# Kernel optimization log

Hardware: AMD Instinct MI355X
Metric: run time of the kernel (lower is better)

## Reference

```python
import jax, jax.numpy as jnp
import numpy as np
import math

B, N, L = 1, 256, 384
D_MSA, D_PAIR, H, DH = 256, 128, 8, 32


def layer_norm(x, g, b, eps=1e-5):
    m = jnp.mean(x, axis=-1, keepdims=True)
    v = jnp.var(x, axis=-1, keepdims=True)
    return (x - m) * jax.lax.rsqrt(v + eps) * g + b


def setup_inputs() -> dict:
    key = jax.random.key(0)
    ks = jax.random.split(key, 16)
    hd = H * DH
    w = lambda k, shp, s=0.05: (jax.random.normal(k, shp, dtype=jnp.float32) * s)
    return {
        "msa": jax.random.normal(ks[0], (B, N, L, D_MSA), dtype=jnp.float32),
        "pair": jax.random.normal(ks[1], (B, L, L, D_PAIR), dtype=jnp.float32),
        "ln_msa_g": jnp.ones((D_MSA,), jnp.float32),
        "ln_msa_b": jnp.zeros((D_MSA,), jnp.float32),
        "ln_pair_g": jnp.ones((D_PAIR,), jnp.float32),
        "ln_pair_b": jnp.zeros((D_PAIR,), jnp.float32),
        "sw_q_w": w(ks[2], (D_MSA, hd)),
        "sw_q_b": jnp.zeros((hd,), jnp.float32),
        "sw_k_w": w(ks[3], (D_MSA, hd)),
        "sw_k_b": jnp.zeros((hd,), jnp.float32),
        "wq": w(ks[4], (D_MSA, hd)),
        "wk": w(ks[5], (D_MSA, hd)),
        "wv": w(ks[6], (D_MSA, hd)),
        "wb": w(ks[7], (D_PAIR, H)),
        "wg": w(ks[8], (D_MSA, hd)),
        "bg": jnp.ones((hd,), jnp.float32),
        "wo": w(ks[9], (hd, D_MSA)),
        "bo": jnp.zeros((D_MSA,), jnp.float32),
    }


def reference(msa, pair, ln_msa_g, ln_msa_b, ln_pair_g, ln_pair_b,
              sw_q_w, sw_q_b, sw_k_w, sw_k_b,
              wq, wk, wv, wb, wg, bg, wo, bo):
    b, n, l, _ = msa.shape
    scale = 1.0 / math.sqrt(DH)

    msa_n = layer_norm(msa, ln_msa_g, ln_msa_b)
    pair_n = layer_norm(pair, ln_pair_g, ln_pair_b)

    # SequenceWeight: attention of target seq (row 0) over all N rows, per (L, head)
    tar = msa_n[:, 0]                                       # [B,L,D]
    swq = (tar @ sw_q_w + sw_q_b).reshape(b, l, H, DH) * scale
    swk = (msa_n @ sw_k_w + sw_k_b).reshape(b, n, l, H, DH)
    sw_logits = jnp.einsum('blhd,bnlhd->bnlh', swq, swk)    # [B,N,L,H]
    seq_weight = jax.nn.softmax(sw_logits, axis=1)          # softmax over N (dropout: eval)

    query = (msa_n @ wq).reshape(b, n, l, H, DH) * seq_weight[..., None]
    key = (msa_n @ wk).reshape(b, n, l, H, DH) * scale
    value = (msa_n @ wv).reshape(b, n, l, H, DH)
    bias = pair_n @ wb                                      # [B,L,L,H]
    gate = jax.nn.sigmoid(msa_n @ wg + bg)                  # [B,N,L,H*DH]

    attn = jnp.einsum('bsqhd,bskhd->bqkh', query, key) + bias
    attn = jax.nn.softmax(attn, axis=-2)                    # over k axis
    out = jnp.einsum('bqkh,bskhd->bsqhd', attn, value).reshape(b, n, l, H * DH)
    out = gate * out
    return out @ wo + bo
```

## Files before the change

### kernel.cpp

```cpp
#include <hip/hip_runtime.h>
#include <hip/hip_fp16.h>
#include <stdint.h>

#define NSEQ 256
#define LSEQ 384
#define DM   256
#define DP   128
#define NH   8
#define DHD  32
#define NL   (NSEQ*LSEQ)
#define LL   (LSEQ*LSEQ)
#define SCALE 0.17677669529663687f

typedef unsigned short u16;
typedef short bf16x8 __attribute__((ext_vector_type(8)));
typedef float f32x4 __attribute__((ext_vector_type(4)));

__device__ __forceinline__ float b2f(u16 s){
  union { uint32_t u; float f; } v; v.u = ((uint32_t)s)<<16; return v.f;
}
__device__ __forceinline__ u16 f2b(float f){
  union { float f; uint32_t u; } v; v.f = f;
  uint32_t u = v.u;
  return (u16)((u + 0x7FFFu + ((u>>16)&1u)) >> 16);
}
__device__ __forceinline__ float wsum(float x){
  #pragma unroll
  for(int o=32;o>0;o>>=1) x += __shfl_xor(x,o,64);
  return x;
}
__device__ __forceinline__ float wmax(float x){
  #pragma unroll
  for(int o=32;o>0;o>>=1) x = fmaxf(x, __shfl_xor(x,o,64));
  return x;
}
__device__ __forceinline__ void gload16(const void* g, void* l){
  __builtin_amdgcn_global_load_lds((const __attribute__((address_space(1))) void*)g,
      (__attribute__((address_space(3))) void*)l, 16, 0, 0);
}

__global__ __launch_bounds__(256) void k_ln_msa(const float* __restrict__ msa,
    const float* __restrict__ g, const float* __restrict__ b, u16* __restrict__ out){
  int lane = threadIdx.x & 63;
  int64_t row = (int64_t)blockIdx.x*4 + (threadIdx.x>>6);
  const float4 x = *(const float4*)(msa + row*DM + lane*4);
  float s = x.x+x.y+x.z+x.w;
  float q = x.x*x.x+x.y*x.y+x.z*x.z+x.w*x.w;
  s = wsum(s); q = wsum(q);
  float mean = s*(1.0f/DM);
  float rstd = rsqrtf(q*(1.0f/DM) - mean*mean + 1e-5f);
  int c = lane*4;
  float4 gv = *(const float4*)(g+c);
  float4 bv = *(const float4*)(b+c);
  ushort4 o;
  o.x=f2b((x.x-mean)*rstd*gv.x+bv.x);
  o.y=f2b((x.y-mean)*rstd*gv.y+bv.y);
  o.z=f2b((x.z-mean)*rstd*gv.z+bv.z);
  o.w=f2b((x.w-mean)*rstd*gv.w+bv.w);
  *(ushort4*)(out + row*DM + c) = o;
}

__global__ __launch_bounds__(256) void k_wconv(const float* __restrict__ wq,
    const float* __restrict__ wk, const float* __restrict__ wv,
    const float* __restrict__ wg, const float* __restrict__ wo,
    u16* __restrict__ WTall, u16* __restrict__ WOT){
  __shared__ float tile[64][65];
  int z = blockIdx.z;
  const float* src = (z==0)?wq:(z==1)?wk:(z==2)?wv:(z==3)?wg:wo;
  u16* dst = (z<4) ? (WTall + z*DM*DM) : WOT;
  int k0 = blockIdx.x*64, n0 = blockIdx.y*64, t = threadIdx.x;
  int r = t>>4, c4 = (t&15)*4;
  #pragma unroll
  for(int it=0; it<4; it++){
    float4 v = *(const float4*)(src + (int64_t)(k0 + it*16 + r)*DM + n0 + c4);
    tile[it*16+r][c4+0]=v.x; tile[it*16+r][c4+1]=v.y;
    tile[it*16+r][c4+2]=v.z; tile[it*16+r][c4+3]=v.w;
  }
  __syncthreads();
  #pragma unroll
  for(int it=0; it<4; it++){
    int nl = it*16 + r, kl = c4;
    ushort4 o;
    o.x=f2b(tile[kl+0][nl]); o.y=f2b(tile[kl+1][nl]);
    o.z=f2b(tile[kl+2][nl]); o.w=f2b(tile[kl+3][nl]);
    *(ushort4*)(dst + (int64_t)(n0+nl)*DM + k0 + kl) = o;
  }
}

__global__ __launch_bounds__(256) void k_u(const u16* __restrict__ msa_n,
    const float* __restrict__ sw_q_w, const float* __restrict__ sw_q_b,
    const float* __restrict__ sw_k_w, float* __restrict__ u){
  __shared__ float tar[DM];
  __shared__ float swq[DM];
  int l = blockIdx.x, t = threadIdx.x;
  tar[t] = b2f(msa_n[(int64_t)l*DM + t]);
  __syncthreads();
  float acc = sw_q_b[t];
  for(int c=0;c<DM;c++) acc += tar[c]*sw_q_w[c*DM + t];
  swq[t] = acc * SCALE;
  __syncthreads();
  float res[NH];
  #pragma unroll
  for(int h=0;h<NH;h++){
    float a = 0.f;
    #pragma unroll
    for(int d=0;d<DHD;d+=4){
      float4 w = *(const float4*)(sw_k_w + t*DM + h*DHD + d);
      a += w.x*swq[h*DHD+d] + w.y*swq[h*DHD+d+1] + w.z*swq[h*DHD+d+2] + w.w*swq[h*DHD+d+3];
    }
    res[h]=a;
  }
  #pragma unroll
  for(int h=0;h<NH;h++) u[((int64_t)l*NH + h)*DM + t] = res[h];
}

__global__ __launch_bounds__(256) void k_seqw(const u16* __restrict__ msa_n,
    const float* __restrict__ u, float* __restrict__ sw){
  __shared__ float ul[NH*DM];
  __shared__ float lg[NH*256];
  __shared__ float mx[NH], sm[NH];
  int l = blockIdx.x, t = threadIdx.x;
  #pragma unroll
  for(int h=0;h<NH;h++) ul[h*DM+t] = u[((int64_t)l*NH+h)*DM + t];
  __syncthreads();
  float acc[NH] = {};
  const u16* row = msa_n + ((int64_t)t*LSEQ + l)*DM;
  for(int c=0;c<DM;c+=4){
    ushort4 xv = *(const ushort4*)(row + c);
    float x0=b2f(xv.x), x1=b2f(xv.y), x2=b2f(xv.z), x3=b2f(xv.w);
    #pragma unroll
    for(int h=0;h<NH;h++)
      acc[h] += x0*ul[h*DM+c] + x1*ul[h*DM+c+1] + x2*ul[h*DM+c+2] + x3*ul[h*DM+c+3];
  }
  #pragma unroll
  for(int h=0;h<NH;h++) lg[h*256+t] = acc[h];
  __syncthreads();
  int wv = t>>6, ln = t&63;
  for(int h=wv; h<NH; h+=4){
    float a=lg[h*256+ln], b=lg[h*256+ln+64], c=lg[h*256+ln+128], d=lg[h*256+ln+192];
    float m = wmax(fmaxf(fmaxf(a,b),fmaxf(c,d)));
    float e = __expf(a-m)+__expf(b-m)+__expf(c-m)+__expf(d-m);
    e = wsum(e);
    if(ln==0){ mx[h]=m; sm[h]=1.f/e; }
  }
  __syncthreads();
  float o[NH];
  #pragma unroll
  for(int h=0;h<NH;h++) o[h] = __expf(acc[h]-mx[h])*sm[h];
  float* dst = sw + ((int64_t)t*LSEQ + l)*NH;
  *(float4*)dst     = make_float4(o[0],o[1],o[2],o[3]);
  *(float4*)(dst+4) = make_float4(o[4],o[5],o[6],o[7]);
}

__global__ __launch_bounds__(256) void k_bias(const float* __restrict__ pair,
    const float* __restrict__ g, const float* __restrict__ b,
    const float* __restrict__ wb, float* __restrict__ bias){
  int64_t row = (int64_t)blockIdx.x*256 + threadIdx.x;
  const float* pr = pair + row*DP;
  uint2 xs[32];
  float s = 0.f, q = 0.f;
  #pragma unroll
  for(int i=0;i<32;i++){
    float4 v = *(const float4*)(pr + i*4);
    s += v.x+v.y+v.z+v.w;
    q += v.x*v.x+v.y*v.y+v.z*v.z+v.w*v.w;
    __half2 p0 = __floats2half2_rn(v.x, v.y);
    __half2 p1 = __floats2half2_rn(v.z, v.w);
    xs[i].x = *(const uint32_t*)&p0;
    xs[i].y = *(const uint32_t*)&p1;
  }
  float mean = s*(1.f/DP);
  float rstd = rsqrtf(q*(1.f/DP) - mean*mean + 1e-5f);
  float acc[NH] = {};
  #pragma unroll
  for(int i=0;i<32;i++){
    __half2 p0 = *(const __half2*)&xs[i].x;
    __half2 p1 = *(const __half2*)&xs[i].y;
    float2 f0 = __half22float2(p0);
    float2 f1 = __half22float2(p1);
    float xv[4] = {f0.x, f0.y, f1.x, f1.y};
    #pragma unroll
    for(int c4=0;c4<4;c4++){
      int c = i*4 + c4;
      float y = (xv[c4]-mean)*rstd*g[c] + b[c];
      #pragma unroll
      for(int h=0;h<NH;h++) acc[h] += y*wb[c*NH+h];
    }
  }
  #pragma unroll
  for(int h=0;h<NH;h++) bias[(int64_t)h*LL + row] = acc[h];
}


__global__ __launch_bounds__(256) void k_projf(const u16* __restrict__ A,
    const u16* __restrict__ WT, u16* __restrict__ qb, u16* __restrict__ kb,
    u16* __restrict__ gbuf, u16* __restrict__ VT,
    const float* __restrict__ sw, const float* __restrict__ bg){
  __shared__ short As[128*64];
  __shared__ short Bs[128*64];
  int t = threadIdx.x;
  int w = t>>6, lane = t&63, ln15 = lane&15, quad = lane>>4;
  int rIn = lane>>3, cch = lane&7;
  int mw = (w>>1)*64, nw = (w&1)*64;
  int bx = blockIdx.x;
  int64_t r0 = (int64_t)bx*128;
  int g = cch ^ rIn;
  for(int nt=0; nt<8; nt++){
    int n0 = nt*128;
    f32x4 acc[4][4] = {};
    for(int it=0; it<4; it++){
      int k0 = it*64;
      __syncthreads();
      #pragma unroll
      for(int ti=0; ti<4; ti++){
        int row = w*32 + ti*8 + rIn;
        gload16(A  + (r0+row)*DM + k0 + g*8, &As[(w*32+ti*8)*64]);
        gload16(WT + (int64_t)(n0+row)*DM + k0 + g*8, &Bs[(w*32+ti*8)*64]);
      }
      __syncthreads();
      #pragma unroll
      for(int kk=0;kk<2;kk++){
        int p = (kk*4+quad) ^ (lane&7);
        bf16x8 af[4], bfv[4];
        #pragma unroll
        for(int i=0;i<4;i++) af[i]  = *(const bf16x8*)&As[(mw+i*16+ln15)*64 + p*8];
        #pragma unroll
        for(int j=0;j<4;j++) bfv[j] = *(const bf16x8*)&Bs[(nw+j*16+ln15)*64 + p*8];
        #pragma unroll
        for(int i=0;i<4;i++)
          #pragma unroll
          for(int j=0;j<4;j++)
            acc[i][j] = __builtin_amdgcn_mfma_f32_16x16x32_bf16(af[i], bfv[j], acc[i][j], 0,0,0);
      }
    }
    int mode = nt>>1;
    int cmb = (nt&1)*128 + nw;
    if(mode==2){
      int s = bx/3, kb3 = (bx%3)*128 + mw;
      #pragma unroll
      for(int j=0;j<4;j++){
        int cm = cmb + j*16 + ln15;
        int hh = cm>>5, d = cm&31;
        #pragma unroll
        for(int i=0;i<4;i++){
          int kpos0 = kb3 + i*16 + quad*4;
          ushort4 o;
          o.x=f2b(acc[i][j][0]); o.y=f2b(acc[i][j][1]);
          o.z=f2b(acc[i][j][2]); o.w=f2b(acc[i][j][3]);
          *(ushort4*)(VT + ((int64_t)(hh*NSEQ+s)*DHD + d)*LSEQ + kpos0) = o;
        }
      }
    } else {
      u16* dst = (mode==0)?qb:(mode==1)?kb:gbuf;
      float bgv[4];
      if(mode==3){
        #pragma unroll
        for(int j=0;j<4;j++) bgv[j] = bg[cmb + j*16 + ln15];
      }
      #pragma unroll
      for(int i=0;i<4;i++)
        #pragma unroll
        for(int reg=0;reg<4;reg++){
          int64_t r = r0 + mw + i*16 + quad*4 + reg;
          #pragma unroll
          for(int j=0;j<4;j++){
            int cm = cmb + j*16 + ln15;
            float v = acc[i][j][reg];
            if(mode==0)      v *= sw[r*NH + (cm>>5)];
            else if(mode==1) v *= SCALE;
            else             v = 1.f/(1.f+__expf(-(v+bgv[j])));
            dst[r*DM + cm] = f2b(v);
          }
        }
    }
  }
}

__global__ __launch_bounds__(256) void k_scores(const u16* __restrict__ Q,
    const u16* __restrict__ K, float* __restrict__ scores){
  __shared__ short As[128*64];
  __shared__ short Bs[128*64];
  int t = threadIdx.x;
  int w = t>>6, lane = t&63, ln15 = lane&15, quad = lane>>4;
  int rIn = lane>>3, cch = lane&7;
  int mw = (w>>1)*64, nw = (w&1)*64;
  int q0 = blockIdx.x*128, k0t = blockIdx.y*128;
  int h = blockIdx.z>>2, sc = blockIdx.z&3;
  int g = cch ^ rIn;
  int s_off = g>>2, d16 = g&3;
  f32x4 acc[4][4] = {};
  for(int i2=0; i2<32; i2++){
    int sb = sc*64 + i2*2 + s_off;
    __syncthreads();
    #pragma unroll
    for(int ti=0; ti<4; ti++){
      int row = w*32 + ti*8 + rIn;
      gload16(Q + ((int64_t)sb*LSEQ + q0 + row)*DM + h*DHD + d16*8, &As[(w*32+ti*8)*64]);
      gload16(K + ((int64_t)sb*LSEQ + k0t + row)*DM + h*DHD + d16*8, &Bs[(w*32+ti*8)*64]);
    }
    __syncthreads();
    #pragma unroll
    for(int kk=0;kk<2;kk++){
      int p = (kk*4+quad) ^ (lane&7);
      bf16x8 af[4], bfv[4];
      #pragma unroll
      for(int i=0;i<4;i++) af[i]  = *(const bf16x8*)&As[(mw+i*16+ln15)*64 + p*8];
      #pragma unroll
      for(int j=0;j<4;j++) bfv[j] = *(const bf16x8*)&Bs[(nw+j*16+ln15)*64 + p*8];
      #pragma unroll
      for(int i=0;i<4;i++)
        #pragma unroll
        for(int j=0;j<4;j++)
          acc[i][j] = __builtin_amdgcn_mfma_f32_16x16x32_bf16(af[i], bfv[j], acc[i][j], 0,0,0);
    }
  }
  int64_t slab = (int64_t)sc*NH*LL;
  #pragma unroll
  for(int i=0;i<4;i++)
    #pragma unroll
    for(int reg=0;reg<4;reg++){
      int q = q0 + mw + i*16 + quad*4 + reg;
      float* rp = scores + slab + ((int64_t)h*LSEQ + q)*LSEQ + k0t + nw + ln15;
      #pragma unroll
      for(int j=0;j<4;j++) rp[j*16] = acc[i][j][reg];
    }
}

__global__ __launch_bounds__(128) void k_softmax(const float* __restrict__ scores,
    const float* __restrict__ bias, u16* __restrict__ Pb){
  int hq = blockIdx.x, t = threadIdx.x;
  int64_t base = (int64_t)hq*LSEQ;
  float v[3];
  #pragma unroll
  for(int i=0;i<3;i++){
    int k = t + i*128;
    float x = bias[base+k];
    x += scores[base+k];
    x += scores[(int64_t)1*NH*LL + base + k];
    x += scores[(int64_t)2*NH*LL + base + k];
    x += scores[(int64_t)3*NH*LL + base + k];
    v[i]=x;
  }
  __shared__ float red[2], red2[2];
  int wv=t>>6, ln=t&63;
  float m = fmaxf(fmaxf(v[0],v[1]),v[2]);
  m = wmax(m);
  if(ln==0) red[wv]=m;
  __syncthreads();
  m = fmaxf(red[0],red[1]);
  float e = __expf(v[0]-m)+__expf(v[1]-m)+__expf(v[2]-m);
  e = wsum(e);
  if(ln==0) red2[wv]=e;
  __syncthreads();
  float inv = 1.f/(red2[0]+red2[1]);
  #pragma unroll
  for(int i=0;i<3;i++) Pb[base + t + i*128] = f2b(__expf(v[i]-m)*inv);
}

__global__ __launch_bounds__(256) void k_pv(const u16* __restrict__ VT,
    const u16* __restrict__ Pb, const u16* __restrict__ gbuf,
    u16* __restrict__ attn){
  __shared__ short As[128*64];
  __shared__ short Bs[128*64];
  int t = threadIdx.x;
  int w = t>>6, lane = t&63, ln15 = lane&15, quad = lane>>4;
  int rIn = lane>>3, cch = lane&7;
  int mw = (w>>1)*64, nw = (w&1)*64;
  int mx = blockIdx.x, ny = blockIdx.y, h = blockIdx.z;
  int g = cch ^ rIn;
  f32x4 acc[4][4] = {};
  for(int it=0; it<6; it++){
    int k0 = it*64;
    __syncthreads();
    #pragma unroll
    for(int ti=0; ti<4; ti++){
      int row = w*32 + ti*8 + rIn;
      gload16(VT + ((int64_t)h*8192 + mx*128 + row)*LSEQ + k0 + g*8, &As[(w*32+ti*8)*64]);
      gload16(Pb + ((int64_t)h*LSEQ + ny*128 + row)*LSEQ + k0 + g*8, &Bs[(w*32+ti*8)*64]);
    }
    __syncthreads();
    #pragma unroll
    for(int kk=0;kk<2;kk++){
      int p = (kk*4+quad) ^ (lane&7);
      bf16x8 af[4], bfv[4];
      #pragma unroll
      for(int i=0;i<4;i++) af[i]  = *(const bf16x8*)&As[(mw+i*16+ln15)*64 + p*8];
      #pragma unroll
      for(int j=0;j<4;j++) bfv[j] = *(const bf16x8*)&Bs[(nw+j*16+ln15)*64 + p*8];
      #pragma unroll
      for(int i=0;i<4;i++)
        #pragma unroll
        for(int j=0;j<4;j++)
          acc[i][j] = __builtin_amdgcn_mfma_f32_16x16x32_bf16(af[i], bfv[j], acc[i][j], 0,0,0);
    }
  }
  #pragma unroll
  for(int i=0;i<4;i++){
    int m0 = mx*128 + mw + i*16 + quad*4;
    int s = m0>>5, d0 = m0&31;
    #pragma unroll
    for(int j=0;j<4;j++){
      int q = ny*128 + nw + j*16 + ln15;
      int64_t base = ((int64_t)s*LSEQ + q)*DM + h*DHD + d0;
      ushort4 gv = *(const ushort4*)(gbuf + base);
      ushort4 o;
      o.x = f2b(acc[i][j][0]*b2f(gv.x));
      o.y = f2b(acc[i][j][1]*b2f(gv.y));
      o.z = f2b(acc[i][j][2]*b2f(gv.z));
      o.w = f2b(acc[i][j][3]*b2f(gv.w));
      *(ushort4*)(attn + base) = o;
    }
  }
}

__global__ __launch_bounds__(256) void k_final(const u16* __restrict__ A,
    const u16* __restrict__ WOT, const float* __restrict__ bo,
    float* __restrict__ out){
  __shared__ short As[128*64];
  __shared__ short Bs[128*64];
  int t = threadIdx.x;
  int w = t>>6, lane = t&63, ln15 = lane&15, quad = lane>>4;
  int rIn = lane>>3, cch = lane&7;
  int mw = (w>>1)*64, nw = (w&1)*64;
  int n0 = blockIdx.x*128;
  int64_t r0 = (int64_t)blockIdx.y*128;
  int g = cch ^ rIn;
  f32x4 acc[4][4] = {};
  for(int it=0; it<4; it++){
    int k0 = it*64;
    __syncthreads();
    #pragma unroll
    for(int ti=0; ti<4; ti++){
      int row = w*32 + ti*8 + rIn;
      gload16(A   + (r0+row)*DM + k0 + g*8, &As[(w*32+ti*8)*64]);
      gload16(WOT + (int64_t)(n0+row)*DM + k0 + g*8, &Bs[(w*32+ti*8)*64]);
    }
    __syncthreads();
    #pragma unroll
    for(int kk=0;kk<2;kk++){
      int p = (kk*4+quad) ^ (lane&7);
      bf16x8 af[4], bfv[4];
      #pragma unroll
      for(int i=0;i<4;i++) af[i]  = *(const bf16x8*)&As[(mw+i*16+ln15)*64 + p*8];
      #pragma unroll
      for(int j=0;j<4;j++) bfv[j] = *(const bf16x8*)&Bs[(nw+j*16+ln15)*64 + p*8];
      #pragma unroll
      for(int i=0;i<4;i++)
        #pragma unroll
        for(int j=0;j<4;j++)
          acc[i][j] = __builtin_amdgcn_mfma_f32_16x16x32_bf16(af[i], bfv[j], acc[i][j], 0,0,0);
    }
  }
  float bv[4];
  #pragma unroll
  for(int j=0;j<4;j++) bv[j] = bo[n0 + nw + j*16 + ln15];
  #pragma unroll
  for(int i=0;i<4;i++)
    #pragma unroll
    for(int reg=0;reg<4;reg++){
      int64_t r = r0 + mw + i*16 + quad*4 + reg;
      float* rp = out + r*DM + n0 + nw + ln15;
      #pragma unroll
      for(int j=0;j<4;j++) rp[j*16] = acc[i][j][reg] + bv[j];
    }
}

extern "C" void kernel_launch(void* const* d_in, const int* in_sizes, int n_in,
                              void* d_out, int out_size, void* d_ws, size_t ws_size,
                              hipStream_t stream){
  const float* msa    = (const float*)d_in[0];
  const float* pair   = (const float*)d_in[1];
  const float* lmg    = (const float*)d_in[2];
  const float* lmb    = (const float*)d_in[3];
  const float* lpg    = (const float*)d_in[4];
  const float* lpb    = (const float*)d_in[5];
  const float* sw_q_w = (const float*)d_in[6];
  const float* sw_q_b = (const float*)d_in[7];
  const float* sw_k_w = (const float*)d_in[8];
  const float* wq     = (const float*)d_in[10];
  const float* wk     = (const float*)d_in[11];
  const float* wv     = (const float*)d_in[12];
  const float* wb     = (const float*)d_in[13];
  const float* wg     = (const float*)d_in[14];
  const float* bg     = (const float*)d_in[15];
  const float* wo     = (const float*)d_in[16];
  const float* bo     = (const float*)d_in[17];
  float* out = (float*)d_out;

  u16* msa_n = (u16*)d_ws;
  u16* qb    = msa_n + (int64_t)NL*DM;
  u16* kb    = qb + (int64_t)NL*DM;
  u16* gbuf  = kb + (int64_t)NL*DM;
  u16* VT    = gbuf + (int64_t)NL*DM;
  u16* Pb    = VT + (int64_t)NL*DM;
  u16* WTall = Pb + (int64_t)NH*LSEQ*LSEQ;
  u16* WOT   = WTall + 1024*DM;
  float* u_buf = (float*)(WOT + DM*DM);
  float* sw  = u_buf + (int64_t)LSEQ*NH*DM;
  float* bias = sw + (int64_t)NL*NH;
  float* scores = bias + (int64_t)NH*LL;
  u16* attnout = msa_n;

  k_ln_msa<<<NL/4, 256, 0, stream>>>(msa, lmg, lmb, msa_n);
  k_wconv<<<dim3(4,4,5), 256, 0, stream>>>(wq, wk, wv, wg, wo, WTall, WOT);
  k_u<<<LSEQ, 256, 0, stream>>>(msa_n, sw_q_w, sw_q_b, sw_k_w, u_buf);
  k_seqw<<<LSEQ, 256, 0, stream>>>(msa_n, u_buf, sw);
  k_bias<<<LL/256, 256, 0, stream>>>(pair, lpg, lpb, wb, bias);
  k_projf<<<dim3(NL/128), 256, 0, stream>>>(msa_n, WTall, qb, kb, gbuf, VT, sw, bg);
  k_scores<<<dim3(3,3,32), 256, 0, stream>>>(qb, kb, scores);
  k_softmax<<<NH*LSEQ, 128, 0, stream>>>(scores, bias, Pb);
  k_pv<<<dim3(64,3,NH), 256, 0, stream>>>(VT, Pb, gbuf, attnout);
  k_final<<<dim3(2, NL/128), 256, 0, stream>>>(attnout, WOT, bo, out);
}
```

Baseline: 730.2 us.

## Double-buffer LDS tiles in all MFMA GEMM kernels to overlap loads with compute

Gives the projection, scores, PV and final-output GEMM kernels two LDS buffers per operand. Each kernel issues the global-to-LDS loads for the next k-step before running the MFMAs on the current one, which removes one barrier per iteration. In the projection kernel the nested n-tile/k loops are flattened into one 32-step stream so prefetching also crosses n-tile boundaries, with the epilogue done every fourth step. LDS use per block doubles to 64 KB, which can lower the number of resident blocks per CU.

```diff
diff --git a/kernel.cpp b/kernel.cpp
--- a/kernel.cpp
+++ b/kernel.cpp
@@ -196,8 +196,8 @@
     const u16* __restrict__ WT, u16* __restrict__ qb, u16* __restrict__ kb,
     u16* __restrict__ gbuf, u16* __restrict__ VT,
     const float* __restrict__ sw, const float* __restrict__ bg){
-  __shared__ short As[128*64];
-  __shared__ short Bs[128*64];
+  __shared__ short As[2][128*64];
+  __shared__ short Bs[2][128*64];
   int t = threadIdx.x;
   int w = t>>6, lane = t&63, ln15 = lane&15, quad = lane>>4;
   int rIn = lane>>3, cch = lane&7;
@@ -205,81 +205,92 @@
   int bx = blockIdx.x;
   int64_t r0 = (int64_t)bx*128;
   int g = cch ^ rIn;
-  for(int nt=0; nt<8; nt++){
-    int n0 = nt*128;
-    f32x4 acc[4][4] = {};
-    for(int it=0; it<4; it++){
-      int k0 = it*64;
-      __syncthreads();
-      #pragma unroll
-      for(int ti=0; ti<4; ti++){
-        int row = w*32 + ti*8 + rIn;
-        gload16(A  + (r0+row)*DM + k0 + g*8, &As[(w*32+ti*8)*64]);
-        gload16(WT + (int64_t)(n0+row)*DM + k0 + g*8, &Bs[(w*32+ti*8)*64]);
-      }
-      __syncthreads();
-      #pragma unroll
-      for(int kk=0;kk<2;kk++){
-        int p = (kk*4+quad) ^ (lane&7);
-        bf16x8 af[4], bfv[4];
-        #pragma unroll
-        for(int i=0;i<4;i++) af[i]  = *(const bf16x8*)&As[(mw+i*16+ln15)*64 + p*8];
-        #pragma unroll
-        for(int j=0;j<4;j++) bfv[j] = *(const bf16x8*)&Bs[(nw+j*16+ln15)*64 + p*8];
+
+  auto PSTAGE = [&](int r, int bsel){
+    int n0_ = (r>>2)*128, k0_ = (r&3)*64;
+    #pragma unroll
+    for(int ti=0; ti<4; ti++){
+      int row = w*32 + ti*8 + rIn;
+      gload16(A  + (r0+row)*DM + k0_ + g*8, &As[bsel][(w*32+ti*8)*64]);
+      gload16(WT + (int64_t)(n0_+row)*DM + k0_ + g*8, &Bs[bsel][(w*32+ti*8)*64]);
+    }
+  };
+
+  f32x4 acc[4][4] = {};
+  PSTAGE(0, 0);
+  __syncthreads();
+  for(int r=0; r<32; r++){
+    int buf = r&1;
+    if(r<31) PSTAGE(r+1, buf^1);
+    #pragma unroll
+    for(int kk=0;kk<2;kk++){
+      int p = (kk*4+quad) ^ (lane&7);
+      bf16x8 af[4], bfv[4];
+      #pragma unroll
+      for(int i=0;i<4;i++) af[i]  = *(const bf16x8*)&As[buf][(mw+i*16+ln15)*64 + p*8];
+      #pragma unroll
+      for(int j=0;j<4;j++) bfv[j] = *(const bf16x8*)&Bs[buf][(nw+j*16+ln15)*64 + p*8];
+      #pragma unroll
+      for(int i=0;i<4;i++)
+        #pragma unroll
+        for(int j=0;j<4;j++)
+          acc[i][j] = __builtin_amdgcn_mfma_f32_16x16x32_bf16(af[i], bfv[j], acc[i][j], 0,0,0);
+    }
+    if((r&3)==3){
+      int nt = r>>2;
+      int mode = nt>>1;
+      int cmb = (nt&1)*128 + nw;
+      if(mode==2){
+        int s = bx/3, kb3 = (bx%3)*128 + mw;
+        #pragma unroll
+        for(int j=0;j<4;j++){
+          int cm = cmb + j*16 + ln15;
+          int hh = cm>>5, d = cm&31;
+          #pragma unroll
+          for(int i=0;i<4;i++){
+            int kpos0 = kb3 + i*16 + quad*4;
+            ushort4 o;
+            o.x=f2b(acc[i][j][0]); o.y=f2b(acc[i][j][1]);
+            o.z=f2b(acc[i][j][2]); o.w=f2b(acc[i][j][3]);
+            *(ushort4*)(VT + ((int64_t)(hh*NSEQ+s)*DHD + d)*LSEQ + kpos0) = o;
+          }
+        }
+      } else {
+        u16* dst = (mode==0)?qb:(mode==1)?kb:gbuf;
+        float bgv[4];
+        if(mode==3){
+          #pragma unroll
+          for(int j=0;j<4;j++) bgv[j] = bg[cmb + j*16 + ln15];
+        }
         #pragma unroll
         for(int i=0;i<4;i++)
           #pragma unroll
-          for(int j=0;j<4;j++)
-            acc[i][j] = __builtin_amdgcn_mfma_f32_16x16x32_bf16(af[i], bfv[j], acc[i][j], 0,0,0);
+          for(int reg=0;reg<4;reg++){
+            int64_t rr = r0 + mw + i*16 + quad*4 + reg;
+            #pragma unroll
+            for(int j=0;j<4;j++){
+              int cm = cmb + j*16 + ln15;
+              float v = acc[i][j][reg];
+              if(mode==0)      v *= sw[rr*NH + (cm>>5)];
+              else if(mode==1) v *= SCALE;
+              else             v = 1.f/(1.f+__expf(-(v+bgv[j])));
+              dst[rr*DM + cm] = f2b(v);
+            }
+          }
       }
-    }
-    int mode = nt>>1;
-    int cmb = (nt&1)*128 + nw;
-    if(mode==2){
-      int s = bx/3, kb3 = (bx%3)*128 + mw;
-      #pragma unroll
-      for(int j=0;j<4;j++){
-        int cm = cmb + j*16 + ln15;
-        int hh = cm>>5, d = cm&31;
-        #pragma unroll
-        for(int i=0;i<4;i++){
-          int kpos0 = kb3 + i*16 + quad*4;
-          ushort4 o;
-          o.x=f2b(acc[i][j][0]); o.y=f2b(acc[i][j][1]);
-          o.z=f2b(acc[i][j][2]); o.w=f2b(acc[i][j][3]);
-          *(ushort4*)(VT + ((int64_t)(hh*NSEQ+s)*DHD + d)*LSEQ + kpos0) = o;
-        }
-      }
-    } else {
-      u16* dst = (mode==0)?qb:(mode==1)?kb:gbuf;
-      float bgv[4];
-      if(mode==3){
-        #pragma unroll
-        for(int j=0;j<4;j++) bgv[j] = bg[cmb + j*16 + ln15];
-      }
       #pragma unroll
       for(int i=0;i<4;i++)
         #pragma unroll
-        for(int reg=0;reg<4;reg++){
-          int64_t r = r0 + mw + i*16 + quad*4 + reg;
-          #pragma unroll
-          for(int j=0;j<4;j++){
-            int cm = cmb + j*16 + ln15;
-            float v = acc[i][j][reg];
-            if(mode==0)      v *= sw[r*NH + (cm>>5)];
-            else if(mode==1) v *= SCALE;
-            else             v = 1.f/(1.f+__expf(-(v+bgv[j])));
-            dst[r*DM + cm] = f2b(v);
-          }
-        }
-    }
+        for(int j=0;j<4;j++) acc[i][j] = (f32x4){0.f,0.f,0.f,0.f};
+    }
+    __syncthreads();
   }
 }
 
 __global__ __launch_bounds__(256) void k_scores(const u16* __restrict__ Q,
     const u16* __restrict__ K, float* __restrict__ scores){
-  __shared__ short As[128*64];
-  __shared__ short Bs[128*64];
+  __shared__ short As[2][128*64];
+  __shared__ short Bs[2][128*64];
   int t = threadIdx.x;
   int w = t>>6, lane = t&63, ln15 = lane&15, quad = lane>>4;
   int rIn = lane>>3, cch = lane&7;
@@ -288,31 +299,38 @@
   int h = blockIdx.z>>2, sc = blockIdx.z&3;
   int g = cch ^ rIn;
   int s_off = g>>2, d16 = g&3;
-  f32x4 acc[4][4] = {};
-  for(int i2=0; i2<32; i2++){
+
+  auto PSTAGE = [&](int i2, int bsel){
     int sb = sc*64 + i2*2 + s_off;
-    __syncthreads();
     #pragma unroll
     for(int ti=0; ti<4; ti++){
       int row = w*32 + ti*8 + rIn;
-      gload16(Q + ((int64_t)sb*LSEQ + q0 + row)*DM + h*DHD + d16*8, &As[(w*32+ti*8)*64]);
-      gload16(K + ((int64_t)sb*LSEQ + k0t + row)*DM + h*DHD + d16*8, &Bs[(w*32+ti*8)*64]);
-    }
-    __syncthreads();
+      gload16(Q + ((int64_t)sb*LSEQ + q0 + row)*DM + h*DHD + d16*8, &As[bsel][(w*32+ti*8)*64]);
+      gload16(K + ((int64_t)sb*LSEQ + k0t + row)*DM + h*DHD + d16*8, &Bs[bsel][(w*32+ti*8)*64]);
+    }
+  };
+
+  f32x4 acc[4][4] = {};
+  PSTAGE(0, 0);
+  __syncthreads();
+  for(int i2=0; i2<32; i2++){
+    int buf = i2&1;
+    if(i2<31) PSTAGE(i2+1, buf^1);
     #pragma unroll
     for(int kk=0;kk<2;kk++){
       int p = (kk*4+quad) ^ (lane&7);
       bf16x8 af[4], bfv[4];
       #pragma unroll
-      for(int i=0;i<4;i++) af[i]  = *(const bf16x8*)&As[(mw+i*16+ln15)*64 + p*8];
-      #pragma unroll
-      for(int j=0;j<4;j++) bfv[j] = *(const bf16x8*)&Bs[(nw+j*16+ln15)*64 + p*8];
+      for(int i=0;i<4;i++) af[i]  = *(const bf16x8*)&As[buf][(mw+i*16+ln15)*64 + p*8];
+      #pragma unroll
+      for(int j=0;j<4;j++) bfv[j] = *(const bf16x8*)&Bs[buf][(nw+j*16+ln15)*64 + p*8];
       #pragma unroll
       for(int i=0;i<4;i++)
         #pragma unroll
         for(int j=0;j<4;j++)
           acc[i][j] = __builtin_amdgcn_mfma_f32_16x16x32_bf16(af[i], bfv[j], acc[i][j], 0,0,0);
     }
+    __syncthreads();
   }
   int64_t slab = (int64_t)sc*NH*LL;
   #pragma unroll
@@ -360,39 +378,46 @@
 __global__ __launch_bounds__(256) void k_pv(const u16* __restrict__ VT,
     const u16* __restrict__ Pb, const u16* __restrict__ gbuf,
     u16* __restrict__ attn){
-  __shared__ short As[128*64];
-  __shared__ short Bs[128*64];
+  __shared__ short As[2][128*64];
+  __shared__ short Bs[2][128*64];
   int t = threadIdx.x;
   int w = t>>6, lane = t&63, ln15 = lane&15, quad = lane>>4;
   int rIn = lane>>3, cch = lane&7;
   int mw = (w>>1)*64, nw = (w&1)*64;
   int mx = blockIdx.x, ny = blockIdx.y, h = blockIdx.z;
   int g = cch ^ rIn;
-  f32x4 acc[4][4] = {};
-  for(int it=0; it<6; it++){
+
+  auto PSTAGE = [&](int it, int bsel){
     int k0 = it*64;
-    __syncthreads();
     #pragma unroll
     for(int ti=0; ti<4; ti++){
       int row = w*32 + ti*8 + rIn;
-      gload16(VT + ((int64_t)h*8192 + mx*128 + row)*LSEQ + k0 + g*8, &As[(w*32+ti*8)*64]);
-      gload16(Pb + ((int64_t)h*LSEQ + ny*128 + row)*LSEQ + k0 + g*8, &Bs[(w*32+ti*8)*64]);
-    }
-    __syncthreads();
+      gload16(VT + ((int64_t)h*8192 + mx*128 + row)*LSEQ + k0 + g*8, &As[bsel][(w*32+ti*8)*64]);
+      gload16(Pb + ((int64_t)h*LSEQ + ny*128 + row)*LSEQ + k0 + g*8, &Bs[bsel][(w*32+ti*8)*64]);
+    }
+  };
+
+  f32x4 acc[4][4] = {};
+  PSTAGE(0, 0);
+  __syncthreads();
+  for(int it=0; it<6; it++){
+    int buf = it&1;
+    if(it<5) PSTAGE(it+1, buf^1);
     #pragma unroll
     for(int kk=0;kk<2;kk++){
       int p = (kk*4+quad) ^ (lane&7);
       bf16x8 af[4], bfv[4];
       #pragma unroll
-      for(int i=0;i<4;i++) af[i]  = *(const bf16x8*)&As[(mw+i*16+ln15)*64 + p*8];
-      #pragma unroll
-      for(int j=0;j<4;j++) bfv[j] = *(const bf16x8*)&Bs[(nw+j*16+ln15)*64 + p*8];
+      for(int i=0;i<4;i++) af[i]  = *(const bf16x8*)&As[buf][(mw+i*16+ln15)*64 + p*8];
+      #pragma unroll
+      for(int j=0;j<4;j++) bfv[j] = *(const bf16x8*)&Bs[buf][(nw+j*16+ln15)*64 + p*8];
       #pragma unroll
       for(int i=0;i<4;i++)
         #pragma unroll
         for(int j=0;j<4;j++)
           acc[i][j] = __builtin_amdgcn_mfma_f32_16x16x32_bf16(af[i], bfv[j], acc[i][j], 0,0,0);
     }
+    __syncthreads();
   }
   #pragma unroll
   for(int i=0;i<4;i++){
@@ -416,8 +441,8 @@
 __global__ __launch_bounds__(256) void k_final(const u16* __restrict__ A,
     const u16* __restrict__ WOT, const float* __restrict__ bo,
     float* __restrict__ out){
-  __shared__ short As[128*64];
-  __shared__ short Bs[128*64];
+  __shared__ short As[2][128*64];
+  __shared__ short Bs[2][128*64];
   int t = threadIdx.x;
   int w = t>>6, lane = t&63, ln15 = lane&15, quad = lane>>4;
   int rIn = lane>>3, cch = lane&7;
@@ -425,31 +450,38 @@
   int n0 = blockIdx.x*128;
   int64_t r0 = (int64_t)blockIdx.y*128;
   int g = cch ^ rIn;
-  f32x4 acc[4][4] = {};
-  for(int it=0; it<4; it++){
+
+  auto PSTAGE = [&](int it, int bsel){
     int k0 = it*64;
-    __syncthreads();
     #pragma unroll
     for(int ti=0; ti<4; ti++){
       int row = w*32 + ti*8 + rIn;
-      gload16(A   + (r0+row)*DM + k0 + g*8, &As[(w*32+ti*8)*64]);
-      gload16(WOT + (int64_t)(n0+row)*DM + k0 + g*8, &Bs[(w*32+ti*8)*64]);
-    }
-    __syncthreads();
+      gload16(A   + (r0+row)*DM + k0 + g*8, &As[bsel][(w*32+ti*8)*64]);
+      gload16(WOT + (int64_t)(n0+row)*DM + k0 + g*8, &Bs[bsel][(w*32+ti*8)*64]);
+    }
+  };
+
+  f32x4 acc[4][4] = {};
+  PSTAGE(0, 0);
+  __syncthreads();
+  for(int it=0; it<4; it++){
+    int buf = it&1;
+    if(it<3) PSTAGE(it+1, buf^1);
     #pragma unroll
     for(int kk=0;kk<2;kk++){
       int p = (kk*4+quad) ^ (lane&7);
       bf16x8 af[4], bfv[4];
       #pragma unroll
-      for(int i=0;i<4;i++) af[i]  = *(const bf16x8*)&As[(mw+i*16+ln15)*64 + p*8];
-      #pragma unroll
-      for(int j=0;j<4;j++) bfv[j] = *(const bf16x8*)&Bs[(nw+j*16+ln15)*64 + p*8];
+      for(int i=0;i<4;i++) af[i]  = *(const bf16x8*)&As[buf][(mw+i*16+ln15)*64 + p*8];
+      #pragma unroll
+      for(int j=0;j<4;j++) bfv[j] = *(const bf16x8*)&Bs[buf][(nw+j*16+ln15)*64 + p*8];
       #pragma unroll
       for(int i=0;i<4;i++)
         #pragma unroll
         for(int j=0;j<4;j++)
           acc[i][j] = __builtin_amdgcn_mfma_f32_16x16x32_bf16(af[i], bfv[j], acc[i][j], 0,0,0);
     }
+    __syncthreads();
   }
   float bv[4];
   #pragma unroll
```

New measurement: 758.8 us. 1.04x slower.

## Keep full-K activation tile resident in LDS and stream weights from global

Applied to the files above, without the earlier changes.

In both the projection GEMM and the final output GEMM, the whole 128x256 activation tile is loaded into shared memory once per block with an XOR swizzle. Weight fragments are then read directly from global/L2 into registers, which removes the per-K-step LDS staging and barriers. The final GEMM now loops over both 128-wide N tiles inside one block, so the activation tile is read once instead of twice. The cost is 64KB of LDS per block, which may lower occupancy, and weight loads become uncoalesced 16-byte global reads with no LDS reuse.

```diff
diff --git a/kernel.cpp b/kernel.cpp
--- a/kernel.cpp
+++ b/kernel.cpp
@@ -196,42 +196,45 @@
     const u16* __restrict__ WT, u16* __restrict__ qb, u16* __restrict__ kb,
     u16* __restrict__ gbuf, u16* __restrict__ VT,
     const float* __restrict__ sw, const float* __restrict__ bg){
-  __shared__ short As[128*64];
-  __shared__ short Bs[128*64];
+  __shared__ short As[128*256];
   int t = threadIdx.x;
   int w = t>>6, lane = t&63, ln15 = lane&15, quad = lane>>4;
-  int rIn = lane>>3, cch = lane&7;
   int mw = (w>>1)*64, nw = (w&1)*64;
   int bx = blockIdx.x;
   int64_t r0 = (int64_t)bx*128;
-  int g = cch ^ rIn;
+
+  {
+    int rowl = lane>>5;
+    int pc = lane&31;
+    #pragma unroll
+    for(int m=0;m<16;m++){
+      int q = w*16+m;
+      int row = 2*q + rowl;
+      int gch = pc ^ (row&7);
+      gload16(A + (r0+row)*DM + gch*8, &As[q*512]);
+    }
+  }
+  __syncthreads();
+
   for(int nt=0; nt<8; nt++){
     int n0 = nt*128;
     f32x4 acc[4][4] = {};
-    for(int it=0; it<4; it++){
-      int k0 = it*64;
-      __syncthreads();
-      #pragma unroll
-      for(int ti=0; ti<4; ti++){
-        int row = w*32 + ti*8 + rIn;
-        gload16(A  + (r0+row)*DM + k0 + g*8, &As[(w*32+ti*8)*64]);
-        gload16(WT + (int64_t)(n0+row)*DM + k0 + g*8, &Bs[(w*32+ti*8)*64]);
+    #pragma unroll
+    for(int ks=0; ks<8; ks++){
+      bf16x8 af[4], bfv[4];
+      #pragma unroll
+      for(int j=0;j<4;j++)
+        bfv[j] = *(const bf16x8*)(WT + (int64_t)(n0+nw+j*16+ln15)*DM + ks*32 + quad*8);
+      #pragma unroll
+      for(int i=0;i<4;i++){
+        int row = mw+i*16+ln15;
+        af[i] = *(const bf16x8*)&As[row*256 + (((ks*4+quad) ^ (ln15&7)))*8];
       }
-      __syncthreads();
-      #pragma unroll
-      for(int kk=0;kk<2;kk++){
-        int p = (kk*4+quad) ^ (lane&7);
-        bf16x8 af[4], bfv[4];
-        #pragma unroll
-        for(int i=0;i<4;i++) af[i]  = *(const bf16x8*)&As[(mw+i*16+ln15)*64 + p*8];
-        #pragma unroll
-        for(int j=0;j<4;j++) bfv[j] = *(const bf16x8*)&Bs[(nw+j*16+ln15)*64 + p*8];
-        #pragma unroll
-        for(int i=0;i<4;i++)
-          #pragma unroll
-          for(int j=0;j<4;j++)
-            acc[i][j] = __builtin_amdgcn_mfma_f32_16x16x32_bf16(af[i], bfv[j], acc[i][j], 0,0,0);
-      }
+      #pragma unroll
+      for(int i=0;i<4;i++)
+        #pragma unroll
+        for(int j=0;j<4;j++)
+          acc[i][j] = __builtin_amdgcn_mfma_f32_16x16x32_bf16(af[i], bfv[j], acc[i][j], 0,0,0);
     }
     int mode = nt>>1;
     int cmb = (nt&1)*128 + nw;
@@ -261,15 +264,15 @@
       for(int i=0;i<4;i++)
         #pragma unroll
         for(int reg=0;reg<4;reg++){
-          int64_t r = r0 + mw + i*16 + quad*4 + reg;
+          int64_t rr = r0 + mw + i*16 + quad*4 + reg;
           #pragma unroll
           for(int j=0;j<4;j++){
             int cm = cmb + j*16 + ln15;
             float v = acc[i][j][reg];
-            if(mode==0)      v *= sw[r*NH + (cm>>5)];
+            if(mode==0)      v *= sw[rr*NH + (cm>>5)];
             else if(mode==1) v *= SCALE;
             else             v = 1.f/(1.f+__expf(-(v+bgv[j])));
-            dst[r*DM + cm] = f2b(v);
+            dst[rr*DM + cm] = f2b(v);
           }
         }
     }
@@ -416,53 +419,58 @@
 __global__ __launch_bounds__(256) void k_final(const u16* __restrict__ A,
     const u16* __restrict__ WOT, const float* __restrict__ bo,
     float* __restrict__ out){
-  __shared__ short As[128*64];
-  __shared__ short Bs[128*64];
+  __shared__ short As[128*256];
   int t = threadIdx.x;
   int w = t>>6, lane = t&63, ln15 = lane&15, quad = lane>>4;
-  int rIn = lane>>3, cch = lane&7;
   int mw = (w>>1)*64, nw = (w&1)*64;
-  int n0 = blockIdx.x*128;
-  int64_t r0 = (int64_t)blockIdx.y*128;
-  int g = cch ^ rIn;
-  f32x4 acc[4][4] = {};
-  for(int it=0; it<4; it++){
-    int k0 = it*64;
-    __syncthreads();
-    #pragma unroll
-    for(int ti=0; ti<4; ti++){
-      int row = w*32 + ti*8 + rIn;
-      gload16(A   + (r0+row)*DM + k0 + g*8, &As[(w*32+ti*8)*64]);
-      gload16(WOT + (int64_t)(n0+row)*DM + k0 + g*8, &Bs[(w*32+ti*8)*64]);
-    }
-    __syncthreads();
-    #pragma unroll
-    for(int kk=0;kk<2;kk++){
-      int p = (kk*4+quad) ^ (lane&7);
+  int64_t r0 = (int64_t)blockIdx.x*128;
+
+  {
+    int rowl = lane>>5;
+    int pc = lane&31;
+    #pragma unroll
+    for(int m=0;m<16;m++){
+      int q = w*16+m;
+      int row = 2*q + rowl;
+      int gch = pc ^ (row&7);
+      gload16(A + (r0+row)*DM + gch*8, &As[q*512]);
+    }
+  }
+  __syncthreads();
+
+  for(int nt=0; nt<2; nt++){
+    int n0 = nt*128;
+    f32x4 acc[4][4] = {};
+    #pragma unroll
+    for(int ks=0; ks<8; ks++){
       bf16x8 af[4], bfv[4];
       #pragma unroll
-      for(int i=0;i<4;i++) af[i]  = *(const bf16x8*)&As[(mw+i*16+ln15)*64 + p*8];
-      #pragma unroll
-      for(int j=0;j<4;j++) bfv[j] = *(const bf16x8*)&Bs[(nw+j*16+ln15)*64 + p*8];
+      for(int j=0;j<4;j++)
+        bfv[j] = *(const bf16x8*)(WOT + (int64_t)(n0+nw+j*16+ln15)*DM + ks*32 + quad*8);
+      #pragma unroll
+      for(int i=0;i<4;i++){
+        int row = mw+i*16+ln15;
+        af[i] = *(const bf16x8*)&As[row*256 + (((ks*4+quad) ^ (ln15&7)))*8];
+      }
       #pragma unroll
       for(int i=0;i<4;i++)
         #pragma unroll
         for(int j=0;j<4;j++)
           acc[i][j] = __builtin_amdgcn_mfma_f32_16x16x32_bf16(af[i], bfv[j], acc[i][j], 0,0,0);
     }
-  }
-  float bv[4];
-  #pragma unroll
-  for(int j=0;j<4;j++) bv[j] = bo[n0 + nw + j*16 + ln15];
-  #pragma unroll
-  for(int i=0;i<4;i++)
-    #pragma unroll
-    for(int reg=0;reg<4;reg++){
-      int64_t r = r0 + mw + i*16 + quad*4 + reg;
-      float* rp = out + r*DM + n0 + nw + ln15;
-      #pragma unroll
-      for(int j=0;j<4;j++) rp[j*16] = acc[i][j][reg] + bv[j];
-    }
+    float bv[4];
+    #pragma unroll
+    for(int j=0;j<4;j++) bv[j] = bo[n0 + nw + j*16 + ln15];
+    #pragma unroll
+    for(int i=0;i<4;i++)
+      #pragma unroll
+      for(int reg=0;reg<4;reg++){
+        int64_t r = r0 + mw + i*16 + quad*4 + reg;
+        float* rp = out + r*DM + n0 + nw + ln15;
+        #pragma unroll
+        for(int j=0;j<4;j++) rp[j*16] = acc[i][j][reg] + bv[j];
+      }
+  }
 }
 
 extern "C" void kernel_launch(void* const* d_in, const int* in_sizes, int n_in,
@@ -510,5 +518,5 @@
   k_scores<<<dim3(3,3,32), 256, 0, stream>>>(qb, kb, scores);
   k_softmax<<<NH*LSEQ, 128, 0, stream>>>(scores, bias, Pb);
   k_pv<<<dim3(64,3,NH), 256, 0, stream>>>(VT, Pb, gbuf, attnout);
-  k_final<<<dim3(2, NL/128), 256, 0, stream>>>(attnout, WOT, bo, out);
-}
+  k_final<<<dim3(NL/128), 256, 0, stream>>>(attnout, WOT, bo, out);
+}
```

Result: no change. 742.0 us (+1.6%).
